# Kernel tuning notes

Hardware: AMD Instinct MI355X
Metric: run time of the kernel (lower is better)

The kernel has to match this reference:

```python
import jax, jax.numpy as jnp
import numpy as np

N = 100_000      # nodes
E = 3_200_000    # edges (before self-loops)
IN_DIM = 256
H1, H2 = 64, 32
OUT_DIM = 40
NEG_SLOPE = 0.2  # PyG GATConv default


def setup_inputs() -> dict:
    key = jax.random.key(0)
    ks = jax.random.split(key, 12)
    s = 0.05
    return {
        "x": jax.random.normal(ks[0], (N, IN_DIM), jnp.float32),
        "edge_index": jax.random.randint(ks[1], (2, E), 0, N, jnp.int32),
        "W1": jax.random.normal(ks[2], (IN_DIM, H1), jnp.float32) * s,
        "att_src1": jax.random.normal(ks[3], (H1,), jnp.float32) * s,
        "att_dst1": jax.random.normal(ks[4], (H1,), jnp.float32) * s,
        "b1": jnp.zeros((H1,), jnp.float32),
        "W2": jax.random.normal(ks[5], (H1, H2), jnp.float32) * s,
        "att_src2": jax.random.normal(ks[6], (H2,), jnp.float32) * s,
        "att_dst2": jax.random.normal(ks[7], (H2,), jnp.float32) * s,
        "b2": jnp.zeros((H2,), jnp.float32),
        "fcW": jax.random.normal(ks[8], (H2, OUT_DIM), jnp.float32) * s,
        "fcb": jnp.zeros((OUT_DIM,), jnp.float32),
    }


def gat_conv(x, src, dst, W, a_src, a_dst, b):
    """Single-head PyG GATConv (concat, heads=1). src/dst already include self-loops."""
    n = x.shape[0]
    h = x @ W                                   # [N, C] projected features (lin has no bias)
    alpha_s = (h * a_src).sum(-1)               # [N]
    alpha_d = (h * a_dst).sum(-1)               # [N]
    logit = jax.nn.leaky_relu(alpha_s[src] + alpha_d[dst], NEG_SLOPE)  # [E']
    # segment softmax over edges grouped by destination node
    m = jax.ops.segment_max(logit, dst, num_segments=n)               # [N]
    e = jnp.exp(logit - m[dst])                                        # [E']
    denom = jax.ops.segment_sum(e, dst, num_segments=n)               # [N]
    alpha = e / denom[dst]                                             # [E']
    out = jax.ops.segment_sum(h[src] * alpha[:, None], dst, num_segments=n)  # [N, C]
    return out + b


def reference(x, edge_index, W1, att_src1, att_dst1, b1, W2, att_src2, att_dst2, b2, fcW, fcb):
    n = x.shape[0]
    # add_self_loops=True (PyG GATConv default)
    loop = jnp.arange(n, dtype=edge_index.dtype)
    src = jnp.concatenate([edge_index[0], loop])
    dst = jnp.concatenate([edge_index[1], loop])
    h = jax.nn.relu(gat_conv(x, src, dst, W1, att_src1, att_dst1, b1))
    emb = jax.nn.relu(gat_conv(h, src, dst, W2, att_src2, att_dst2, b2))
    logits = emb @ fcW + fcb
    return emb, logits
```

## Files before the change

### kernel.cpp

```cpp
#include <hip/hip_runtime.h>
#include <hip/hip_bf16.h>

#define NEG_SLOPE 0.2f
#define IN_DIM 256
#define C1 64
#define C2 32
#define ODIM 40
#define SCAN_CHUNK 4096
#define BSHIFT 12
#define ECHUNK 8192
#define ECH2 16384
#define CH 10
#define SRCMASK 0x1FFFF

typedef unsigned short ushort16;

__device__ __forceinline__ unsigned bf16_rne(float f) {
    unsigned a = __float_as_uint(f);
    return (a + 0x7FFFu + ((a >> 16) & 1u)) >> 16;
}
__device__ __forceinline__ void bf16x2_unpack(unsigned u, float& f0, float& f1) {
    f0 = __uint_as_float(u << 16);
    f1 = __uint_as_float(u & 0xFFFF0000u);
}


__global__ void k_bhist(const int* __restrict__ dst, int E, int* __restrict__ gh,
                        int nblk, int nb) {
    __shared__ int h[32];
    int t = threadIdx.x;
    if (t < 32) h[t] = 0;
    __syncthreads();
    int base = blockIdx.x * ECHUNK;
    int end = min(base + ECHUNK, E);
    for (int i = base + t; i < end; i += 256) atomicAdd(&h[dst[i] >> BSHIFT], 1);
    __syncthreads();
    if (t < nb) gh[t * nblk + blockIdx.x] = h[t];
}

__global__ void k_bscan(int* __restrict__ gh, int L) {
    __shared__ int lds[256];
    __shared__ int carry;
    int t = threadIdx.x;
    if (t == 0) carry = 0;
    __syncthreads();
    for (int base = 0; base < L; base += 256) {
        int v = (base + t < L) ? gh[base + t] : 0;
        lds[t] = v; __syncthreads();
        for (int off = 1; off < 256; off <<= 1) {
            int u = (t >= off) ? lds[t - off] : 0;
            __syncthreads();
            lds[t] += u;
            __syncthreads();
        }
        if (base + t < L) gh[base + t] = lds[t] - v + carry;
        __syncthreads();
        if (t == 0) carry += lds[255];
        __syncthreads();
    }
}

__global__ __launch_bounds__(256)
void k_bplace(const int* __restrict__ src, const int* __restrict__ dst, int E,
              const int* __restrict__ gh, int nblk, int nb,
              unsigned* __restrict__ pairs) {
    __shared__ int cnt32[32], lofs[33], lcur[32], delta[32];
    __shared__ unsigned buf[ECHUNK];
    int t = threadIdx.x;
    if (t < 32) cnt32[t] = 0;
    __syncthreads();
    int base = blockIdx.x * ECHUNK;
    int end = min(base + ECHUNK, E);
    for (int i = base + t; i < end; i += 256) atomicAdd(&cnt32[dst[i] >> BSHIFT], 1);
    __syncthreads();
    if (t == 0) {
        int s = 0;
        for (int b = 0; b < 32; b++) { lofs[b] = s; s += cnt32[b]; }
        lofs[32] = s;
    }
    __syncthreads();
    if (t < 32) {
        lcur[t] = lofs[t];
        delta[t] = (t < nb) ? (gh[t * nblk + blockIdx.x] - lofs[t]) : 0;
    }
    __syncthreads();
    for (int i = base + t; i < end; i += 256) {
        int d = dst[i];
        int b = d >> BSHIFT;
        int p = atomicAdd(&lcur[b], 1);
        buf[p] = (unsigned)src[i] | ((unsigned)(d & 4095) << 17);
    }
    __syncthreads();
    int m = end - base;
    for (int j = t; j < m; j += 256) {
        int lo = 0, hi = 31;
        while (lo < hi) { int mid = (lo + hi + 1) >> 1; if (lofs[mid] <= j) lo = mid; else hi = mid - 1; }
        pairs[j + delta[lo]] = buf[j];
    }
}

__device__ __forceinline__ void bc_map(int blk, int* b, int* c) {
    int xcd = blk & 7, k = blk >> 3;
    *b = (k & 3) * 8 + xcd;
    *c = k >> 2;
}

__global__ __launch_bounds__(512)
void k_nhist(const unsigned* __restrict__ pairs, const int* __restrict__ gh, int nblk,
             int nb, int E, int* __restrict__ chist) {
    __shared__ int h[4096];
    int b, c; bc_map(blockIdx.x, &b, &c);
    if (b >= nb) return;
    for (int i = threadIdx.x; i < 4096; i += 512) h[i] = 0;
    __syncthreads();
    int estart = gh[b * nblk];
    int eend = (b + 1 < nb) ? gh[(b + 1) * nblk] : E;
    int s0 = estart + c * ECH2;
    int s1 = min(s0 + ECH2, eend);
    for (int i = s0 + threadIdx.x; i < s1; i += 512)
        atomicAdd(&h[(pairs[i] >> 17) & 4095], 1);
    __syncthreads();
    int* out = chist + ((size_t)b * CH + c) * 4096;
    for (int i = threadIdx.x; i < 4096; i += 512) out[i] = h[i];
}

__global__ void k_cnt(const int* __restrict__ chist, int* __restrict__ cnt, int n) {
    int i = blockIdx.x * 256 + threadIdx.x;
    if (i >= n) return;
    int b = i >> BSHIFT, j = i & 4095;
    const int* p = chist + ((size_t)b * CH) * 4096 + j;
    int s = 1;
#pragma unroll
    for (int c = 0; c < CH; c++) s += p[c * 4096];
    cnt[i] = s;
}

__global__ void k_scan1(const int* __restrict__ cnt, int n, int* __restrict__ bsums) {
    __shared__ int lds[256];
    int t = threadIdx.x;
    int base = blockIdx.x * SCAN_CHUNK + t * 16;
    int s = 0;
#pragma unroll
    for (int i = 0; i < 16; i++) { int idx = base + i; s += (idx < n) ? cnt[idx] : 0; }
    lds[t] = s; __syncthreads();
    for (int off = 128; off > 0; off >>= 1) {
        if (t < off) lds[t] += lds[t + off];
        __syncthreads();
    }
    if (t == 0) bsums[blockIdx.x] = lds[0];
}

__global__ void k_scan2(int* bsums, int nb, int* row_ptr, int n, int total) {
    __shared__ int lds[256];
    int t = threadIdx.x;
    int v = (t < nb) ? bsums[t] : 0;
    lds[t] = v; __syncthreads();
    for (int off = 1; off < 256; off <<= 1) {
        int u = (t >= off) ? lds[t - off] : 0;
        __syncthreads();
        lds[t] += u;
        __syncthreads();
    }
    if (t < nb) bsums[t] = lds[t] - v;
    if (t == 0) row_ptr[n] = total;
}

__global__ void k_scan3(const int* __restrict__ cnt, int n, const int* __restrict__ bsums,
                        int* __restrict__ row_ptr) {
    __shared__ int lds[256];
    int t = threadIdx.x;
    int base = blockIdx.x * SCAN_CHUNK + t * 16;
    int loc[16];
    int s = 0;
#pragma unroll
    for (int i = 0; i < 16; i++) {
        int idx = base + i;
        int c = (idx < n) ? cnt[idx] : 0;
        loc[i] = s; s += c;
    }
    lds[t] = s; __syncthreads();
    for (int off = 1; off < 256; off <<= 1) {
        int u = (t >= off) ? lds[t - off] : 0;
        __syncthreads();
        lds[t] += u;
        __syncthreads();
    }
    int texcl = lds[t] - s + bsums[blockIdx.x];
#pragma unroll
    for (int i = 0; i < 16; i++) {
        int idx = base + i;
        if (idx < n) row_ptr[idx] = texcl + loc[i];
    }
}

__global__ void k_selfloop(const int* __restrict__ row_ptr, int n, int* __restrict__ adj) {
    int i = blockIdx.x * 256 + threadIdx.x;
    if (i < n) adj[row_ptr[i]] = i;
}

__global__ void k_nscan(int* __restrict__ chist, const int* __restrict__ row_ptr, int n) {
    int i = blockIdx.x * 256 + threadIdx.x;
    if (i >= n) return;
    int b = i >> BSHIFT, j = i & 4095;
    int* p = chist + ((size_t)b * CH) * 4096 + j;
    int s = row_ptr[i] + 1;
#pragma unroll
    for (int c = 0; c < CH; c++) { int t = p[c * 4096]; p[c * 4096] = s; s += t; }
}

__global__ __launch_bounds__(512)
void k_place2(const unsigned* __restrict__ pairs, const int* __restrict__ gh, int nblk,
              int nb, int E, const int* __restrict__ chist, int* __restrict__ adj,
              int bbase) {
    __shared__ int cur[4096];
    int b, c; bc_map(blockIdx.x, &b, &c);
    if (b >= nb) return;
    const int* cs = chist + ((size_t)b * CH + c) * 4096;
    for (int i = threadIdx.x; i < 4096; i += 512) cur[i] = cs[i];
    __syncthreads();
    int estart = gh[b * nblk];
    int eend = (b + 1 < nb) ? gh[(b + 1) * nblk] : E;
    int s0 = estart + c * ECH2;
    int s1 = min(s0 + ECH2, eend);
    int nbase = b << BSHIFT; (void)nbase; (void)bbase;
    for (int i = s0 + threadIdx.x; i < s1; i += 512) {
        unsigned p = pairs[i];
        int pos = atomicAdd(&cur[(p >> 17) & 4095], 1);
        adj[pos] = (int)(p & SRCMASK);
    }
}


__global__ __launch_bounds__(256, 4)
void k_gemm1(const float* __restrict__ x, const float* __restrict__ W1,
             const float* __restrict__ attS, const float* __restrict__ attD,
             ushort16* __restrict__ h1b, float* __restrict__ asP,
             float* __restrict__ adP, int n) {
    int t = threadIdx.x;
    int wave = t >> 6, lane = t & 63;
    int half = blockIdx.x & 1;
    int chalf = half * 32;
    int row = (blockIdx.x >> 1) * 256 + wave * 64 + lane;
    bool active = row < n;
    int rowc = active ? row : n - 1;
    const float4* xr = (const float4*)(x + (size_t)rowc * IN_DIM);

    float acc[32];
#pragma unroll
    for (int c = 0; c < 32; c++) acc[c] = 0.f;

#define FMA_K(XC, KK) { \
        const float* wk = wb + (KK) * C1; \
        _Pragma("unroll") \
        for (int c = 0; c < 32; c++) acc[c] = fmaf((XC), wk[c], acc[c]); }

    for (int k0 = 0; k0 < 16; k0++) {
        float4 xv0 = xr[k0 * 4 + 0];
        float4 xv1 = xr[k0 * 4 + 1];
        float4 xv2 = xr[k0 * 4 + 2];
        float4 xv3 = xr[k0 * 4 + 3];
        const float* wb = W1 + (size_t)(k0 * 16) * C1 + chalf;
        FMA_K(xv0.x, 0)  FMA_K(xv0.y, 1)  FMA_K(xv0.z, 2)  FMA_K(xv0.w, 3)
        FMA_K(xv1.x, 4)  FMA_K(xv1.y, 5)  FMA_K(xv1.z, 6)  FMA_K(xv1.w, 7)
        FMA_K(xv2.x, 8)  FMA_K(xv2.y, 9)  FMA_K(xv2.z, 10) FMA_K(xv2.w, 11)
        FMA_K(xv3.x, 12) FMA_K(xv3.y, 13) FMA_K(xv3.z, 14) FMA_K(xv3.w, 15)
    }
#undef FMA_K

    if (!active) return;
    float vs = 0.f, vd = 0.f;
#pragma unroll
    for (int c = 0; c < 32; c++) {
        vs = fmaf(acc[c], attS[chalf + c], vs);
        vd = fmaf(acc[c], attD[chalf + c], vd);
    }
    asP[half * n + row] = vs;
    adP[half * n + row] = vd;

    uint4* hp = (uint4*)((ushort16*)h1b + (size_t)row * C1 + chalf);
#pragma unroll
    for (int j = 0; j < 4; j++) {
        unsigned p0 = bf16_rne(acc[j*8+0]) | (bf16_rne(acc[j*8+1]) << 16);
        unsigned p1 = bf16_rne(acc[j*8+2]) | (bf16_rne(acc[j*8+3]) << 16);
        unsigned p2 = bf16_rne(acc[j*8+4]) | (bf16_rne(acc[j*8+5]) << 16);
        unsigned p3 = bf16_rne(acc[j*8+6]) | (bf16_rne(acc[j*8+7]) << 16);
        hp[j] = make_uint4(p0, p1, p2, p3);
    }
}

__global__ void k_alphaC(const float* __restrict__ asP, const float* __restrict__ adP,
                         float* __restrict__ as1, float* __restrict__ ad1, int n) {
    int i = blockIdx.x * 256 + threadIdx.x;
    if (i < n) {
        as1[i] = asP[i] + asP[(size_t)n + i];
        ad1[i] = adP[i] + adP[(size_t)n + i];
    }
}


__global__ __launch_bounds__(256)
void k_agg1(const ushort16* __restrict__ h1b, const float* __restrict__ as1,
            const float* __restrict__ ad1, const int* __restrict__ row_ptr,
            const int* __restrict__ adj, const float* __restrict__ b1,
            float* __restrict__ h1out, int n) {
    int wave = (blockIdx.x * 256 + threadIdx.x) >> 6;
    int lane = threadIdx.x & 63;
    if (wave >= n) return;
    int d = wave;
    int beg = row_ptr[d], end = row_ptr[d + 1];
    float adv = ad1[d];
    int g = lane >> 3, cq = lane & 7;
    float acc[8];
#pragma unroll
    for (int k = 0; k < 8; k++) acc[k] = 0.f;
    float dsum = 0.f;

#define AGG1_ROUND(E_) { \
        int se = __shfl(s, (E_)); \
        float we = __shfl(w, (E_)); \
        uint4 u = ((const uint4*)(h1b + (size_t)se * C1))[cq]; \
        float f0, f1; \
        bf16x2_unpack(u.x, f0, f1); acc[0]=fmaf(we,f0,acc[0]); acc[1]=fmaf(we,f1,acc[1]); \
        bf16x2_unpack(u.y, f0, f1); acc[2]=fmaf(we,f0,acc[2]); acc[3]=fmaf(we,f1,acc[3]); \
        bf16x2_unpack(u.z, f0, f1); acc[4]=fmaf(we,f0,acc[4]); acc[5]=fmaf(we,f1,acc[5]); \
        bf16x2_unpack(u.w, f0, f1); acc[6]=fmaf(we,f0,acc[6]); acc[7]=fmaf(we,f1,acc[7]); }

    for (int base = beg; base < end; base += 64) {
        int cnt = min(64, end - base);
        int s = d; float w = 0.f;
        if (lane < cnt) {
            s = adj[base + lane];
            float lg = as1[s] + adv;
            lg = lg > 0.f ? lg : NEG_SLOPE * lg;
            w = expf(lg);
            dsum += w;
        }
        int j = 0;
        for (; j + 32 <= cnt; j += 32) {
            AGG1_ROUND(j + g)
            AGG1_ROUND(j + 8 + g)
            AGG1_ROUND(j + 16 + g)
            AGG1_ROUND(j + 24 + g)
        }
        for (; j < cnt; j += 8) AGG1_ROUND(j + g)
    }
#undef AGG1_ROUND

#pragma unroll
    for (int off = 32; off > 0; off >>= 1) dsum += __shfl_xor(dsum, off);
#pragma unroll
    for (int off = 8; off <= 32; off <<= 1) {
#pragma unroll
        for (int k = 0; k < 8; k++) acc[k] += __shfl_xor(acc[k], off);
    }
    if (g == 0) {
        float inv = 1.f / dsum;
        float4 bv0 = ((const float4*)b1)[cq * 2];
        float4 bv1 = ((const float4*)b1)[cq * 2 + 1];
        float4 o0, o1;
        o0.x = acc[0] * inv + bv0.x; o0.x = o0.x > 0.f ? o0.x : 0.f;
        o0.y = acc[1] * inv + bv0.y; o0.y = o0.y > 0.f ? o0.y : 0.f;
        o0.z = acc[2] * inv + bv0.z; o0.z = o0.z > 0.f ? o0.z : 0.f;
        o0.w = acc[3] * inv + bv0.w; o0.w = o0.w > 0.f ? o0.w : 0.f;
        o1.x = acc[4] * inv + bv1.x; o1.x = o1.x > 0.f ? o1.x : 0.f;
        o1.y = acc[5] * inv + bv1.y; o1.y = o1.y > 0.f ? o1.y : 0.f;
        o1.z = acc[6] * inv + bv1.z; o1.z = o1.z > 0.f ? o1.z : 0.f;
        o1.w = acc[7] * inv + bv1.w; o1.w = o1.w > 0.f ? o1.w : 0.f;
        float4* op = (float4*)(h1out + (size_t)d * C1 + cq * 8);
        op[0] = o0; op[1] = o1;
    }
}


__global__ __launch_bounds__(256)
void k_gemm2(const float* __restrict__ h1out, const float* __restrict__ W2,
             const float* __restrict__ attS, const float* __restrict__ attD,
             ushort16* __restrict__ h2b, float* __restrict__ as2,
             float* __restrict__ ad2, int n) {
    __shared__ float w2t[C2 * 68];
    __shared__ float sAttS[C2], sAttD[C2];
    int t = threadIdx.x;
    for (int i = t; i < C1 * C2; i += 256) {
        int k = i >> 5, c = i & 31;
        w2t[c * 68 + k] = W2[i];
    }
    if (t < C2) { sAttS[t] = attS[t]; sAttD[t] = attD[t]; }
    __syncthreads();
    int wave = t >> 6, lane = t & 63;
    int col = lane & 31, half = lane >> 5;
    int rowbase = blockIdx.x * 32 + wave * 8;
    const float* wrow = &w2t[col * 68];
    for (int rr = 0; rr < 8; rr += 2) {
        int row = rowbase + rr + half;
        if (row >= n) return;
        float acc = 0.f;
#pragma unroll
        for (int k = 0; k < C1; k += 4) {
            float4 wv = *(const float4*)&wrow[k];
            float4 xv = *(const float4*)&h1out[(size_t)row * C1 + k];
            acc = fmaf(xv.x, wv.x, acc);
            acc = fmaf(xv.y, wv.y, acc);
            acc = fmaf(xv.z, wv.z, acc);
            acc = fmaf(xv.w, wv.w, acc);
        }
        h2b[(size_t)row * C2 + col] = (ushort16)bf16_rne(acc);
        float vs = acc * sAttS[col], vd = acc * sAttD[col];
#pragma unroll
        for (int off = 16; off > 0; off >>= 1) {
            vs += __shfl_xor(vs, off);
            vd += __shfl_xor(vd, off);
        }
        if (col == 0) { as2[row] = vs; ad2[row] = vd; }
    }
}


__global__ __launch_bounds__(256)
void k_agg2(const ushort16* __restrict__ h2b, const float* __restrict__ as2,
            const float* __restrict__ ad2, const int* __restrict__ row_ptr,
            const int* __restrict__ adj, const float* __restrict__ b2,
            float* __restrict__ emb, int n) {
    int wave = (blockIdx.x * 256 + threadIdx.x) >> 6;
    int lane = threadIdx.x & 63;
    if (wave >= n) return;
    int d = wave;
    int beg = row_ptr[d], end = row_ptr[d + 1];
    float adv = ad2[d];
    int g = lane >> 2, cq = lane & 3;
    float acc[8];
#pragma unroll
    for (int k = 0; k < 8; k++) acc[k] = 0.f;
    float dsum = 0.f;

#define AGG2_ROUND(E_) { \
        int se = __shfl(s, (E_)); \
        float we = __shfl(w, (E_)); \
        uint4 u = ((const uint4*)(h2b + (size_t)se * C2))[cq]; \
        float f0, f1; \
        bf16x2_unpack(u.x, f0, f1); acc[0]=fmaf(we,f0,acc[0]); acc[1]=fmaf(we,f1,acc[1]); \
        bf16x2_unpack(u.y, f0, f1); acc[2]=fmaf(we,f0,acc[2]); acc[3]=fmaf(we,f1,acc[3]); \
        bf16x2_unpack(u.z, f0, f1); acc[4]=fmaf(we,f0,acc[4]); acc[5]=fmaf(we,f1,acc[5]); \
        bf16x2_unpack(u.w, f0, f1); acc[6]=fmaf(we,f0,acc[6]); acc[7]=fmaf(we,f1,acc[7]); }

    for (int base = beg; base < end; base += 64) {
        int cnt = min(64, end - base);
        int s = d; float w = 0.f;
        if (lane < cnt) {
            s = adj[base + lane];
            float lg = as2[s] + adv;
            lg = lg > 0.f ? lg : NEG_SLOPE * lg;
            w = expf(lg);
            dsum += w;
        }
        int j = 0;
        for (; j + 64 <= cnt; j += 64) {
            AGG2_ROUND(j + g)
            AGG2_ROUND(j + 16 + g)
            AGG2_ROUND(j + 32 + g)
            AGG2_ROUND(j + 48 + g)
        }
        for (; j < cnt; j += 16) AGG2_ROUND(j + g)
    }
#undef AGG2_ROUND

#pragma unroll
    for (int off = 32; off > 0; off >>= 1) dsum += __shfl_xor(dsum, off);
#pragma unroll
    for (int off = 4; off <= 32; off <<= 1) {
#pragma unroll
        for (int k = 0; k < 8; k++) acc[k] += __shfl_xor(acc[k], off);
    }
    if (g == 0) {
        float inv = 1.f / dsum;
        float4 bv0 = ((const float4*)b2)[cq * 2];
        float4 bv1 = ((const float4*)b2)[cq * 2 + 1];
        float4 o0, o1;
        o0.x = acc[0] * inv + bv0.x; o0.x = o0.x > 0.f ? o0.x : 0.f;
        o0.y = acc[1] * inv + bv0.y; o0.y = o0.y > 0.f ? o0.y : 0.f;
        o0.z = acc[2] * inv + bv0.z; o0.z = o0.z > 0.f ? o0.z : 0.f;
        o0.w = acc[3] * inv + bv0.w; o0.w = o0.w > 0.f ? o0.w : 0.f;
        o1.x = acc[4] * inv + bv1.x; o1.x = o1.x > 0.f ? o1.x : 0.f;
        o1.y = acc[5] * inv + bv1.y; o1.y = o1.y > 0.f ? o1.y : 0.f;
        o1.z = acc[6] * inv + bv1.z; o1.z = o1.z > 0.f ? o1.z : 0.f;
        o1.w = acc[7] * inv + bv1.w; o1.w = o1.w > 0.f ? o1.w : 0.f;
        float4* op = (float4*)(emb + (size_t)d * C2 + cq * 8);
        op[0] = o0; op[1] = o1;
    }
}


__global__ __launch_bounds__(256)
void k_logits(const float* __restrict__ emb, const float* __restrict__ fcW,
              const float* __restrict__ fcb, float* __restrict__ out, int n) {
    __shared__ float w[C2 * ODIM];
    __shared__ float b[ODIM];
    int t = threadIdx.x;
    for (int i = t; i < C2 * ODIM; i += 256) w[i] = fcW[i];
    if (t < ODIM) b[t] = fcb[t];
    __syncthreads();
    int lane = t & 63;
    int row = blockIdx.x * 4 + (t >> 6);
    if (row >= n) return;
    float acc = (lane < ODIM) ? b[lane] : 0.f;
    const float4* er = (const float4*)&emb[(size_t)row * C2];
#pragma unroll
    for (int c4 = 0; c4 < 8; c4++) {
        float4 e = er[c4];
        int c = c4 * 4;
        if (lane < ODIM) {
            acc = fmaf(e.x, w[(c + 0) * ODIM + lane], acc);
            acc = fmaf(e.y, w[(c + 1) * ODIM + lane], acc);
            acc = fmaf(e.z, w[(c + 2) * ODIM + lane], acc);
            acc = fmaf(e.w, w[(c + 3) * ODIM + lane], acc);
        }
    }
    if (lane < ODIM) out[(size_t)row * ODIM + lane] = acc;
}


extern "C" void kernel_launch(void* const* d_in, const int* in_sizes, int n_in,
                              void* d_out, int out_size, void* d_ws, size_t ws_size,
                              hipStream_t stream) {
    const float* x    = (const float*)d_in[0];
    const int*   ei   = (const int*)d_in[1];
    const float* W1   = (const float*)d_in[2];
    const float* aS1  = (const float*)d_in[3];
    const float* aD1  = (const float*)d_in[4];
    const float* b1   = (const float*)d_in[5];
    const float* W2   = (const float*)d_in[6];
    const float* aS2  = (const float*)d_in[7];
    const float* aD2  = (const float*)d_in[8];
    const float* b2   = (const float*)d_in[9];
    const float* fcW  = (const float*)d_in[10];
    const float* fcb  = (const float*)d_in[11];

    const int N = in_sizes[0] / IN_DIM;
    const int E = in_sizes[1] / 2;
    const int* src = ei;
    const int* dst = ei + E;

    ushort16* h1b = (ushort16*)d_ws;
    float* h1out  = (float*)((char*)d_ws + (size_t)N * C1 * 2);
    float* as1    = h1out + (size_t)N * C1;
    float* ad1    = as1 + N;
    float* as2    = ad1 + N;
    float* ad2    = as2 + N;
    float* asP    = ad2 + N;
    float* adP    = asP + 2 * (size_t)N;
    int*   cnt    = (int*)(adP + 2 * (size_t)N);
    int*   row_ptr = cnt + N;
    int*   bsums   = row_ptr + (N + 1);
    int*   adj     = bsums + 256;
    int*   gh      = adj + (E + N);

    unsigned* pairs = (unsigned*)h1out;
    int*  chist = (int*)h1b;
    ushort16* h2b = (ushort16*)h1b;

    float* emb    = (float*)d_out;
    float* logits = emb + (size_t)N * C2;

    int nbN   = (N + 255) / 256;
    int nbS   = (N + SCAN_CHUNK - 1) / SCAN_CHUNK;
    int nblkE = (E + ECHUNK - 1) / ECHUNK;
    int nb    = (N + (1 << BSHIFT) - 1) >> BSHIFT;
    int nBC   = 8 * 4 * CH;

    k_bhist<<<nblkE, 256, 0, stream>>>(dst, E, gh, nblkE, nb);
    k_bscan<<<1, 256, 0, stream>>>(gh, nb * nblkE);
    k_bplace<<<nblkE, 256, 0, stream>>>(src, dst, E, gh, nblkE, nb, pairs);
    k_nhist<<<nBC, 512, 0, stream>>>(pairs, gh, nblkE, nb, E, chist);
    k_cnt<<<nbN, 256, 0, stream>>>(chist, cnt, N);
    k_scan1<<<nbS, 256, 0, stream>>>(cnt, N, bsums);
    k_scan2<<<1, 256, 0, stream>>>(bsums, nbS, row_ptr, N, E + N);
    k_scan3<<<nbS, 256, 0, stream>>>(cnt, N, bsums, row_ptr);
    k_selfloop<<<nbN, 256, 0, stream>>>(row_ptr, N, adj);
    k_nscan<<<nbN, 256, 0, stream>>>(chist, row_ptr, N);
    k_place2<<<nBC, 512, 0, stream>>>(pairs, gh, nblkE, nb, E, chist, adj, 0);

    int nbG1 = 2 * ((N + 255) / 256);
    k_gemm1<<<nbG1, 256, 0, stream>>>(x, W1, aS1, aD1, h1b, asP, adP, N);
    k_alphaC<<<nbN, 256, 0, stream>>>(asP, adP, as1, ad1, N);
    int nbA = (N + 3) / 4;
    k_agg1<<<nbA, 256, 0, stream>>>(h1b, as1, ad1, row_ptr, adj, b1, h1out, N);
    int nbG2 = (N + 31) / 32;
    k_gemm2<<<nbG2, 256, 0, stream>>>(h1out, W2, aS2, aD2, h2b, as2, ad2, N);
    k_agg2<<<nbA, 256, 0, stream>>>(h2b, as2, ad2, row_ptr, adj, b2, emb, N);
    k_logits<<<nbA, 256, 0, stream>>>(emb, fcW, fcb, logits, N);
}
```

Before: 421.8 us.

## Parallelize bucket-histogram scan, double CSR placement chunks, fuse self-loop into nscan

Replaces the single-block serial scan of the bucket histogram with a three-kernel multi-block scan (reduce, scan of block sums, downsweep), so the L = nb*nblkE entries are no longer scanned by one workgroup. It also halves the per-block edge chunk in the node histogram and placement kernels (CH 10 to 20), doubling their block count for more parallelism at the cost of more chist storage and scan work per node. The self-loop write is folded into k_nscan to drop one launch. The chist buffer aliases h1b, so its size must still fit within N*C1*2 bytes.

```diff
diff --git a/kernel.cpp b/kernel.cpp
--- a/kernel.cpp
+++ b/kernel.cpp
@@ -9,8 +9,8 @@
 #define SCAN_CHUNK 4096
 #define BSHIFT 12
 #define ECHUNK 8192
-#define ECH2 16384
-#define CH 10
+#define ECH2 8192
+#define CH 20
 #define SRCMASK 0x1FFFF
 
 typedef unsigned short ushort16;
@@ -38,25 +38,59 @@
     if (t < nb) gh[t * nblk + blockIdx.x] = h[t];
 }
 
-__global__ void k_bscan(int* __restrict__ gh, int L) {
+__global__ void k_gs1(const int* __restrict__ gh, int L, int* __restrict__ gsums) {
     __shared__ int lds[256];
-    __shared__ int carry;
-    int t = threadIdx.x;
-    if (t == 0) carry = 0;
-    __syncthreads();
-    for (int base = 0; base < L; base += 256) {
-        int v = (base + t < L) ? gh[base + t] : 0;
-        lds[t] = v; __syncthreads();
-        for (int off = 1; off < 256; off <<= 1) {
-            int u = (t >= off) ? lds[t - off] : 0;
-            __syncthreads();
-            lds[t] += u;
-            __syncthreads();
-        }
-        if (base + t < L) gh[base + t] = lds[t] - v + carry;
-        __syncthreads();
-        if (t == 0) carry += lds[255];
-        __syncthreads();
+    int t = threadIdx.x;
+    int base = blockIdx.x * SCAN_CHUNK + t * 16;
+    int s = 0;
+#pragma unroll
+    for (int i = 0; i < 16; i++) { int idx = base + i; s += (idx < L) ? gh[idx] : 0; }
+    lds[t] = s; __syncthreads();
+    for (int off = 128; off > 0; off >>= 1) {
+        if (t < off) lds[t] += lds[t + off];
+        __syncthreads();
+    }
+    if (t == 0) gsums[blockIdx.x] = lds[0];
+}
+
+__global__ void k_gs2(int* __restrict__ gsums, int nblks) {
+    __shared__ int lds[256];
+    int t = threadIdx.x;
+    int v = (t < nblks) ? gsums[t] : 0;
+    lds[t] = v; __syncthreads();
+    for (int off = 1; off < 256; off <<= 1) {
+        int u = (t >= off) ? lds[t - off] : 0;
+        __syncthreads();
+        lds[t] += u;
+        __syncthreads();
+    }
+    if (t < nblks) gsums[t] = lds[t] - v;
+}
+
+__global__ void k_gs3(int* __restrict__ gh, int L, const int* __restrict__ gsums) {
+    __shared__ int lds[256];
+    int t = threadIdx.x;
+    int base = blockIdx.x * SCAN_CHUNK + t * 16;
+    int loc[16];
+    int s = 0;
+#pragma unroll
+    for (int i = 0; i < 16; i++) {
+        int idx = base + i;
+        int c = (idx < L) ? gh[idx] : 0;
+        loc[i] = s; s += c;
+    }
+    lds[t] = s; __syncthreads();
+    for (int off = 1; off < 256; off <<= 1) {
+        int u = (t >= off) ? lds[t - off] : 0;
+        __syncthreads();
+        lds[t] += u;
+        __syncthreads();
+    }
+    int texcl = lds[t] - s + gsums[blockIdx.x];
+#pragma unroll
+    for (int i = 0; i < 16; i++) {
+        int idx = base + i;
+        if (idx < L) gh[idx] = texcl + loc[i];
     }
 }
 
@@ -193,25 +227,22 @@
     }
 }
 
-__global__ void k_selfloop(const int* __restrict__ row_ptr, int n, int* __restrict__ adj) {
-    int i = blockIdx.x * 256 + threadIdx.x;
-    if (i < n) adj[row_ptr[i]] = i;
-}
-
-__global__ void k_nscan(int* __restrict__ chist, const int* __restrict__ row_ptr, int n) {
+__global__ void k_nscan(int* __restrict__ chist, const int* __restrict__ row_ptr,
+                        int* __restrict__ adj, int n) {
     int i = blockIdx.x * 256 + threadIdx.x;
     if (i >= n) return;
+    int rp = row_ptr[i];
+    adj[rp] = i;
     int b = i >> BSHIFT, j = i & 4095;
     int* p = chist + ((size_t)b * CH) * 4096 + j;
-    int s = row_ptr[i] + 1;
+    int s = rp + 1;
 #pragma unroll
     for (int c = 0; c < CH; c++) { int t = p[c * 4096]; p[c * 4096] = s; s += t; }
 }
 
 __global__ __launch_bounds__(512)
 void k_place2(const unsigned* __restrict__ pairs, const int* __restrict__ gh, int nblk,
-              int nb, int E, const int* __restrict__ chist, int* __restrict__ adj,
-              int bbase) {
+              int nb, int E, const int* __restrict__ chist, int* __restrict__ adj) {
     __shared__ int cur[4096];
     int b, c; bc_map(blockIdx.x, &b, &c);
     if (b >= nb) return;
@@ -222,7 +253,6 @@
     int eend = (b + 1 < nb) ? gh[(b + 1) * nblk] : E;
     int s0 = estart + c * ECH2;
     int s1 = min(s0 + ECH2, eend);
-    int nbase = b << BSHIFT; (void)nbase; (void)bbase;
     for (int i = s0 + threadIdx.x; i < s1; i += 512) {
         unsigned p = pairs[i];
         int pos = atomicAdd(&cur[(p >> 17) & 4095], 1);
@@ -550,7 +580,8 @@
     int*   cnt    = (int*)(adP + 2 * (size_t)N);
     int*   row_ptr = cnt + N;
     int*   bsums   = row_ptr + (N + 1);
-    int*   adj     = bsums + 256;
+    int*   gsums   = bsums + 256;
+    int*   adj     = gsums + 256;
     int*   gh      = adj + (E + N);
 
     unsigned* pairs = (unsigned*)h1out;
@@ -564,19 +595,22 @@
     int nbS   = (N + SCAN_CHUNK - 1) / SCAN_CHUNK;
     int nblkE = (E + ECHUNK - 1) / ECHUNK;
     int nb    = (N + (1 << BSHIFT) - 1) >> BSHIFT;
-    int nBC   = 8 * 4 * CH;
+    int nBC   = 32 * CH;
+    int L     = nb * nblkE;
+    int nbG   = (L + SCAN_CHUNK - 1) / SCAN_CHUNK;
 
     k_bhist<<<nblkE, 256, 0, stream>>>(dst, E, gh, nblkE, nb);
-    k_bscan<<<1, 256, 0, stream>>>(gh, nb * nblkE);
+    k_gs1<<<nbG, 256, 0, stream>>>(gh, L, gsums);
+    k_gs2<<<1, 256, 0, stream>>>(gsums, nbG);
+    k_gs3<<<nbG, 256, 0, stream>>>(gh, L, gsums);
     k_bplace<<<nblkE, 256, 0, stream>>>(src, dst, E, gh, nblkE, nb, pairs);
     k_nhist<<<nBC, 512, 0, stream>>>(pairs, gh, nblkE, nb, E, chist);
     k_cnt<<<nbN, 256, 0, stream>>>(chist, cnt, N);
     k_scan1<<<nbS, 256, 0, stream>>>(cnt, N, bsums);
     k_scan2<<<1, 256, 0, stream>>>(bsums, nbS, row_ptr, N, E + N);
     k_scan3<<<nbS, 256, 0, stream>>>(cnt, N, bsums, row_ptr);
-    k_selfloop<<<nbN, 256, 0, stream>>>(row_ptr, N, adj);
-    k_nscan<<<nbN, 256, 0, stream>>>(chist, row_ptr, N);
-    k_place2<<<nBC, 512, 0, stream>>>(pairs, gh, nblkE, nb, E, chist, adj, 0);
+    k_nscan<<<nbN, 256, 0, stream>>>(chist, row_ptr, adj, N);
+    k_place2<<<nBC, 512, 0, stream>>>(pairs, gh, nblkE, nb, E, chist, adj);
 
     int nbG1 = 2 * ((N + 255) / 256);
     k_gemm1<<<nbG1, 256, 0, stream>>>(x, W1, aS1, aD1, h1b, asP, adP, N);
```

Measured after the change: 387.7 us. -8.1%, faster.
